# Performance work log

Hardware: AMD Instinct MI355X
Metric: run time of the kernel (lower is better)

Reference implementation:

```python
import jax, jax.numpy as jnp
import numpy as np


def _dot_prod_attention(h, enc):
    # h: (B,T,H), enc: (B,S,H) used as both keys and values
    att = jnp.einsum('bth,bsh->bts', h, enc)      # (B,T,S)
    att = jax.nn.softmax(att, axis=-1)
    ctx = jnp.einsum('bts,bsh->bth', att, enc)    # (B,T,H)
    return ctx, att


def setup_inputs() -> dict:
    key = jax.random.key(0)
    ks = jax.random.split(key, 7)
    B, T, S, St, H = 8, 1024, 1024, 512, 1024
    scale = 1.0 / np.sqrt(H)
    return {
        'output': jax.random.normal(ks[0], (B, T, H), dtype=jnp.float32),
        'sent': jax.random.normal(ks[1], (B, S, H), dtype=jnp.float32),
        'template': jax.random.normal(ks[2], (B, St, H), dtype=jnp.float32),
        'W_gate': jax.random.normal(ks[3], (H, 3 * H), dtype=jnp.float32) * scale,
        'W_sent': jax.random.normal(ks[4], (H, H), dtype=jnp.float32) * scale,
        'W_template': jax.random.normal(ks[5], (H, H), dtype=jnp.float32) * scale,
        'W_output': jax.random.normal(ks[6], (H, H), dtype=jnp.float32) * scale,
    }


def reference(output, sent, template, W_gate, W_sent, W_template, W_output):
    sent_ctx, sent_weight = _dot_prod_attention(output, sent)
    template_ctx, template_weight = _dot_prod_attention(output, template)

    cat = jnp.concatenate([sent_ctx, template_ctx, output], axis=-1)  # (B,T,3H)
    gate = jax.nn.sigmoid(jnp.einsum('btk,hk->bth', cat, W_gate))     # (B,T,H)

    fusion = ((1.0 - gate) * jnp.einsum('bth,kh->btk', sent_ctx, W_sent)
              + gate * jnp.einsum('bth,kh->btk', template_ctx, W_template)
              + jnp.einsum('bth,kh->btk', output, W_output))
    fusion = jnp.tanh(fusion)
    return fusion, sent_weight, template_weight
```

## Files before the change

### kernel.cpp

```cpp
#include <hip/hip_runtime.h>
#include <stdint.h>

typedef unsigned short u16;
typedef float    f32x4 __attribute__((ext_vector_type(4)));
typedef _Float16 f16x8 __attribute__((ext_vector_type(8)));
typedef _Float16 f16x4 __attribute__((ext_vector_type(4)));

__device__ __forceinline__ u16 f2h(float f) {
  _Float16 h = (_Float16)f;
  u16 u; __builtin_memcpy(&u, &h, 2); return u;
}
__device__ __forceinline__ float h2f(u16 u) {
  _Float16 h; __builtin_memcpy(&h, &u, 2); return (float)h;
}

__device__ __forceinline__ void mfma_f16(f32x4& c, f16x8 a, f16x8 b) {
  c = __builtin_amdgcn_mfma_f32_16x16x32_f16(a, b, c, 0, 0, 0);
}

__device__ __forceinline__ void g2l16(const u16* g, u16* l) {
  __builtin_amdgcn_global_load_lds((const __attribute__((address_space(1))) void*)g,
                                   (__attribute__((address_space(3))) void*)l,
                                   16, 0, 0);
}

__device__ __forceinline__ void xcd_batch(int& bx, int& by, int& bz) {
  const int gx = gridDim.x, gy = gridDim.y;
  const int n = gx * gy * gridDim.z;
  const int lin = blockIdx.x + gx * (blockIdx.y + gy * blockIdx.z);
  const int q = n >> 3;
  const int s = (lin & 7) * q + (lin >> 3);
  bx = s % gx;
  const int t2 = s / gx;
  by = t2 % gy;
  bz = t2 / gy;
}

__device__ __forceinline__ void xcd_col(int& bx, int& by) {
  const int gx = gridDim.x, gy = gridDim.y;
  const int n = gx * gy;
  const int cpx = n >> 3;
  const int lin = blockIdx.x + gx * blockIdx.y;
  const int s = (lin & 7) * cpx + (lin >> 3);
  bx = s / gy;
  by = s % gy;
}

struct alignas(8) US4 { u16 a, b, c, d; };

__global__ void k_conv_hilo(const float* __restrict__ src, u16* __restrict__ hi,
                            u16* __restrict__ lo, int n4) {
  int i = blockIdx.x * blockDim.x + threadIdx.x;
  int stride = gridDim.x * blockDim.x;
  for (; i < n4; i += stride) {
    float4 v = reinterpret_cast<const float4*>(src)[i];
    US4 h, l;
    h.a = f2h(v.x); l.a = f2h(v.x - h2f(h.a));
    h.b = f2h(v.y); l.b = f2h(v.y - h2f(h.b));
    h.c = f2h(v.z); l.c = f2h(v.z - h2f(h.c));
    h.d = f2h(v.w); l.d = f2h(v.w - h2f(h.d));
    reinterpret_cast<US4*>(hi)[i] = h;
    reinterpret_cast<US4*>(lo)[i] = l;
  }
}

__global__ void k_conv_w(const float* __restrict__ s_wg, const float* __restrict__ s_ws,
                         const float* __restrict__ s_wt, const float* __restrict__ s_wo,
                         u16* __restrict__ d_wg, u16* __restrict__ d_ws,
                         u16* __restrict__ d_wt, u16* __restrict__ d_wo) {
  constexpr int N1 = 786432;
  constexpr int N2 = 262144;
  constexpr int total = N1 + 3 * N2;
  int i = blockIdx.x * blockDim.x + threadIdx.x;
  int stride = gridDim.x * blockDim.x;
  for (; i < total; i += stride) {
    const float* s; u16* d; int j;
    if (i < N1)                { s = s_wg; d = d_wg; j = i; }
    else if (i < N1 + N2)      { s = s_ws; d = d_ws; j = i - N1; }
    else if (i < N1 + 2 * N2)  { s = s_wt; d = d_wt; j = i - N1 - N2; }
    else                       { s = s_wo; d = d_wo; j = i - N1 - 2 * N2; }
    float4 v = reinterpret_cast<const float4*>(s)[j];
    US4 h; h.a = f2h(v.x); h.b = f2h(v.y); h.c = f2h(v.z); h.d = f2h(v.w);
    reinterpret_cast<US4*>(d)[j] = h;
  }
}

__global__ __launch_bounds__(256)
void k_conv_T(const float* __restrict__ src, u16* __restrict__ dh, u16* __restrict__ dl,
              u16* __restrict__ dt, int R, int C) {
  __shared__ u16 t[32][33];
  const int b = blockIdx.z;
  const float* s = src + (size_t)b * R * C;
  u16* dhb = dh + (size_t)b * R * C;
  u16* dlb = dl + (size_t)b * R * C;
  u16* dtb = dt + (size_t)b * R * C;
  const int c0 = blockIdx.x * 32, r0 = blockIdx.y * 32;
  const int tx = threadIdx.x, ty = threadIdx.y;
#pragma unroll
  for (int j = ty; j < 32; j += 8) {
    const size_t idx = (size_t)(r0 + j) * C + (c0 + tx);
    float x = s[idx];
    u16 h = f2h(x);
    dhb[idx] = h;
    dlb[idx] = f2h(x - h2f(h));
    t[j][tx] = h;
  }
  __syncthreads();
#pragma unroll
  for (int j = ty; j < 32; j += 8)
    dtb[(size_t)(c0 + j) * R + (r0 + tx)] = t[tx][j];
}

template<int L>
__global__ __launch_bounds__(256)
void k_softmax(float* __restrict__ io, u16* __restrict__ pb) {
  const int lane = threadIdx.x & 63;
  const size_t r = (size_t)blockIdx.x * 4 + (threadIdx.x >> 6);
  float* row = io + r * L;
  u16* prow = pb + r * L;
  constexpr int NV = L / 64;
  float v[NV];
  float mx = -3.4e38f;
#pragma unroll
  for (int j = 0; j < NV; ++j) { v[j] = row[lane + j * 64]; mx = fmaxf(mx, v[j]); }
#pragma unroll
  for (int s = 32; s; s >>= 1) mx = fmaxf(mx, __shfl_xor(mx, s));
  float sum = 0.f;
#pragma unroll
  for (int j = 0; j < NV; ++j) { v[j] = __expf(v[j] - mx); sum += v[j]; }
#pragma unroll
  for (int s = 32; s; s >>= 1) sum += __shfl_xor(sum, s);
  const float inv = 1.f / sum;
#pragma unroll
  for (int j = 0; j < NV; ++j) {
    float pv = v[j] * inv;
    row[lane + j * 64] = pv;
    prow[lane + j * 64] = f2h(pv);
  }
}

struct TC { int wv, sr, sc, wm, wn, fr, kq; };

__device__ __forceinline__ TC make_tc(int tid) {
  TC t;
  const int lane = tid & 63;
  t.wv = tid >> 6;
  t.sr = lane >> 2;
  t.sc = (lane & 3) * 8;
  t.wm = t.wv >> 1;
  t.wn = t.wv & 1;
  t.fr = lane & 15;
  t.kq = (lane >> 4) * 8;
  return t;
}

constexpr int SUB = 128 * 32;

__device__ __forceinline__ void pass64(
    f32x4 (&acc)[16],
    const u16* __restrict__ A, int lda,
    const u16* __restrict__ B, int ldb,
    int K, u16* sA, u16* sB, const TC& t)
{
  const int nt = K / 64;
  auto stage = [&](int c, int k0) {
#pragma unroll
    for (int sub = 0; sub < 2; ++sub) {
      u16* dA = sA + c * (2 * SUB) + sub * SUB;
      u16* dB = sB + c * (2 * SUB) + sub * SUB;
      const u16* ar = A + (size_t)t.sr * lda + k0 + sub * 32 + t.sc;
      const u16* br = B + (size_t)t.sr * ldb + k0 + sub * 32 + t.sc;
      g2l16(ar + (size_t)(t.wv * 16) * lda, dA + (t.wv * 16) * 32);
      g2l16(ar + (size_t)((t.wv + 4) * 16) * lda, dA + ((t.wv + 4) * 16) * 32);
      g2l16(br + (size_t)(t.wv * 16) * ldb, dB + (t.wv * 16) * 32);
      g2l16(br + (size_t)((t.wv + 4) * 16) * ldb, dB + ((t.wv + 4) * 16) * 32);
    }
  };

  stage(0, 0);
  __syncthreads();
  int c = 0;
  for (int it = 0; it < nt; ++it) {
    if (it + 1 < nt) stage(c ^ 1, (it + 1) * 64);
#pragma unroll
    for (int sub = 0; sub < 2; ++sub) {
      const u16* bA = sA + c * (2 * SUB) + sub * SUB;
      const u16* bB = sB + c * (2 * SUB) + sub * SUB;
      f16x8 ah[4], bh[4];
#pragma unroll
      for (int i = 0; i < 4; ++i) {
        ah[i] = *reinterpret_cast<const f16x8*>(&bA[(t.wm * 64 + i * 16 + t.fr) * 32 + t.kq]);
        bh[i] = *reinterpret_cast<const f16x8*>(&bB[(t.wn * 64 + i * 16 + t.fr) * 32 + t.kq]);
      }
#pragma unroll
      for (int i = 0; i < 4; ++i)
#pragma unroll
        for (int j = 0; j < 4; ++j)
          mfma_f16(acc[i * 4 + j], ah[i], bh[j]);
    }
    __syncthreads();
    c ^= 1;
  }
}

__device__ __forceinline__ void pass32s(
    f32x4 (&acc)[16],
    const u16* __restrict__ A, const u16* __restrict__ Al, int lda,
    const u16* __restrict__ B, const u16* __restrict__ Bl, int ldb,
    int K, u16* sA, u16* sAl, u16* sB, u16* sBl, const TC& t)
{
  const int nt = K / 32;
  auto stage = [&](int c, int k0) {
    u16* dA = sA + c * SUB;  u16* dB = sB + c * SUB;
    u16* dAl = sAl + c * SUB; u16* dBl = sBl + c * SUB;
    const u16* ar = A + (size_t)t.sr * lda + k0 + t.sc;
    const u16* br = B + (size_t)t.sr * ldb + k0 + t.sc;
    const u16* alr = Al + (size_t)t.sr * lda + k0 + t.sc;
    const u16* blr = Bl + (size_t)t.sr * ldb + k0 + t.sc;
    g2l16(ar + (size_t)(t.wv * 16) * lda, dA + (t.wv * 16) * 32);
    g2l16(ar + (size_t)((t.wv + 4) * 16) * lda, dA + ((t.wv + 4) * 16) * 32);
    g2l16(br + (size_t)(t.wv * 16) * ldb, dB + (t.wv * 16) * 32);
    g2l16(br + (size_t)((t.wv + 4) * 16) * ldb, dB + ((t.wv + 4) * 16) * 32);
    g2l16(alr + (size_t)(t.wv * 16) * lda, dAl + (t.wv * 16) * 32);
    g2l16(alr + (size_t)((t.wv + 4) * 16) * lda, dAl + ((t.wv + 4) * 16) * 32);
    g2l16(blr + (size_t)(t.wv * 16) * ldb, dBl + (t.wv * 16) * 32);
    g2l16(blr + (size_t)((t.wv + 4) * 16) * ldb, dBl + ((t.wv + 4) * 16) * 32);
  };

  stage(0, 0);
  __syncthreads();
  int c = 0;
  for (int it = 0; it < nt; ++it) {
    if (it + 1 < nt) stage(c ^ 1, (it + 1) * 32);
    const u16* bA = sA + c * SUB;  const u16* bB = sB + c * SUB;
    const u16* bAl = sAl + c * SUB; const u16* bBl = sBl + c * SUB;
    f16x8 ah[4], bh[4], al[4], bl[4];
#pragma unroll
    for (int i = 0; i < 4; ++i) {
      ah[i] = *reinterpret_cast<const f16x8*>(&bA[(t.wm * 64 + i * 16 + t.fr) * 32 + t.kq]);
      bh[i] = *reinterpret_cast<const f16x8*>(&bB[(t.wn * 64 + i * 16 + t.fr) * 32 + t.kq]);
      al[i] = *reinterpret_cast<const f16x8*>(&bAl[(t.wm * 64 + i * 16 + t.fr) * 32 + t.kq]);
      bl[i] = *reinterpret_cast<const f16x8*>(&bBl[(t.wn * 64 + i * 16 + t.fr) * 32 + t.kq]);
    }
#pragma unroll
    for (int i = 0; i < 4; ++i)
#pragma unroll
      for (int j = 0; j < 4; ++j) {
        mfma_f16(acc[i * 4 + j], ah[i], bh[j]);
        mfma_f16(acc[i * 4 + j], al[i], bh[j]);
        mfma_f16(acc[i * 4 + j], ah[i], bl[j]);
      }
    __syncthreads();
    c ^= 1;
  }
}

__global__ __launch_bounds__(256, 2)
void k_logits(const u16* __restrict__ Ah, const u16* __restrict__ Al,
              const u16* __restrict__ Bh, const u16* __restrict__ Bl,
              long long strB, float* __restrict__ Cf, int ldc, long long strC)
{
  __shared__ __align__(16) u16 sA[2 * SUB], sB[2 * SUB], sAl[2 * SUB], sBl[2 * SUB];
  int bx, by, bz;
  xcd_batch(bx, by, bz);
  const TC t = make_tc(threadIdx.x);

  const size_t aoff = (size_t)bz * (1024 * 1024) + (size_t)by * 128 * 1024;
  const size_t boff = (size_t)bz * strB + (size_t)bx * 128 * 1024;

  f32x4 acc[16];
#pragma unroll
  for (int i = 0; i < 16; ++i) acc[i] = f32x4{0.f, 0.f, 0.f, 0.f};

  pass32s(acc, Ah + aoff, Al + aoff, 1024, Bh + boff, Bl + boff, 1024, 1024,
          sA, sAl, sB, sBl, t);

  const size_t cbse = (size_t)bz * strC;
  const int row0 = by * 128 + t.wm * 64;
  const int col0 = bx * 128 + t.wn * 64;
  const int fq = ((threadIdx.x & 63) >> 4) * 4;
#pragma unroll
  for (int i = 0; i < 4; ++i)
#pragma unroll
    for (int j = 0; j < 4; ++j) {
      const int c = col0 + j * 16 + t.fr;
#pragma unroll
      for (int q = 0; q < 4; ++q)
        Cf[cbse + (size_t)(row0 + i * 16 + fq + q) * ldc + c] = acc[i * 4 + j][q];
    }
}

__global__ __launch_bounds__(256, 2)
void k_pv(const u16* __restrict__ A, const u16* __restrict__ Bt, int ld,
          long long strA, long long strB, u16* __restrict__ Cb, long long strC)
{
  __shared__ __align__(16) u16 sA[2 * 2 * SUB], sB[2 * 2 * SUB];
  int bx, by, bz;
  xcd_batch(bx, by, bz);
  const TC t = make_tc(threadIdx.x);

  f32x4 acc[16];
#pragma unroll
  for (int i = 0; i < 16; ++i) acc[i] = f32x4{0.f, 0.f, 0.f, 0.f};

  pass64(acc, A + (size_t)bz * strA + (size_t)by * 128 * ld, ld,
         Bt + (size_t)bz * strB + (size_t)bx * 128 * ld, ld, ld, sA, sB, t);

  const size_t cbse = (size_t)bz * strC;
  const int row0 = by * 128 + t.wm * 64;
  const int col0 = bx * 128 + t.wn * 64;
  const int fq = ((threadIdx.x & 63) >> 4) * 4;
#pragma unroll
  for (int i = 0; i < 4; ++i)
#pragma unroll
    for (int j = 0; j < 4; ++j) {
      const int c = col0 + j * 16 + t.fr;
#pragma unroll
      for (int q = 0; q < 4; ++q)
        Cb[cbse + (size_t)(row0 + i * 16 + fq + q) * 1024 + c] = f2h(acc[i * 4 + j][q]);
    }
}

__global__ __launch_bounds__(256, 2)
void k_fusion4(const u16* __restrict__ ctx_s, const u16* __restrict__ ctx_t,
               const u16* __restrict__ outh,
               const u16* __restrict__ Wg, const u16* __restrict__ Ws,
               const u16* __restrict__ Wt, const u16* __restrict__ Wo,
               float* __restrict__ fus)
{
  constexpr int H = 1024;
  __shared__ __align__(16) u16 sA[2 * 2 * SUB], sB[2 * 2 * SUB];

  int bx, by;
  xcd_col(bx, by);
  const TC t = make_tc(threadIdx.x);

  const size_t aoff = (size_t)by * 128 * H;
  const int row0 = by * 128 + t.wm * 64;
  const int col0 = bx * 128 + t.wn * 64;
  const int fq = ((threadIdx.x & 63) >> 4) * 4;

  f32x4 acc[16];
#pragma unroll
  for (int i = 0; i < 16; ++i) acc[i] = f32x4{0.f, 0.f, 0.f, 0.f};

  const u16* As[3] = {ctx_s, ctx_t, outh};
  for (int s = 0; s < 3; ++s)
    pass64(acc, As[s] + aoff, H, Wg + (size_t)bx * 128 * (3 * H) + s * H, 3 * H, H,
           sA, sB, t);
  f16x4 gh[16];
#pragma unroll
  for (int f = 0; f < 16; ++f)
#pragma unroll
    for (int q = 0; q < 4; ++q)
      gh[f][q] = (_Float16)(1.f / (1.f + __expf(-acc[f][q])));

#pragma unroll
  for (int i = 0; i < 16; ++i) acc[i] = f32x4{0.f, 0.f, 0.f, 0.f};
  pass64(acc, ctx_s + aoff, H, Ws + (size_t)bx * 128 * H, H, H, sA, sB, t);
  f32x4 S[16];
#pragma unroll
  for (int i = 0; i < 16; ++i) { S[i] = acc[i]; acc[i] = f32x4{0.f, 0.f, 0.f, 0.f}; }

  pass64(acc, ctx_t + aoff, H, Wt + (size_t)bx * 128 * H, H, H, sA, sB, t);
#pragma unroll
  for (int f = 0; f < 16; ++f)
#pragma unroll
    for (int q = 0; q < 4; ++q) {
      const float gv = (float)gh[f][q];
      const float sv = S[f][q];
      S[f][q] = sv + gv * (acc[f][q] - sv);
    }
#pragma unroll
  for (int i = 0; i < 16; ++i) acc[i] = f32x4{0.f, 0.f, 0.f, 0.f};

  pass64(acc, outh + aoff, H, Wo + (size_t)bx * 128 * H, H, H, sA, sB, t);
#pragma unroll
  for (int i = 0; i < 4; ++i)
#pragma unroll
    for (int j = 0; j < 4; ++j) {
      const int c = col0 + j * 16 + t.fr;
#pragma unroll
      for (int q = 0; q < 4; ++q) {
        const int r = row0 + i * 16 + fq + q;
        float x = S[i * 4 + j][q] + acc[i * 4 + j][q];
        float ax = fabsf(x);
        float e = __expf(-2.f * ax);
        float th = (1.f - e) / (1.f + e);
        fus[(size_t)r * H + c] = copysignf(th, x);
      }
    }
}

extern "C" void kernel_launch(void* const* d_in, const int* in_sizes, int n_in,
                              void* d_out, int out_size, void* d_ws, size_t ws_size,
                              hipStream_t stream) {
  (void)in_sizes; (void)n_in; (void)out_size; (void)ws_size;
  constexpr int B = 8, T = 1024, S = 1024, St = 512, H = 1024;
  constexpr long long BTH = (long long)B * T * H;
  constexpr long long BSH = (long long)B * S * H;
  constexpr long long BStH = (long long)B * St * H;
  constexpr long long BTS = (long long)B * T * S;
  constexpr long long BTSt = (long long)B * T * St;
  constexpr long long TH = (long long)T * H;

  const float* in_out  = (const float*)d_in[0];
  const float* in_sent = (const float*)d_in[1];
  const float* in_tmpl = (const float*)d_in[2];
  const float* in_Wg   = (const float*)d_in[3];
  const float* in_Ws   = (const float*)d_in[4];
  const float* in_Wt   = (const float*)d_in[5];
  const float* in_Wo   = (const float*)d_in[6];

  float* fus = (float*)d_out;
  float* sw  = fus + BTH;
  float* tw  = sw + BTS;

  char* p = (char*)d_ws;
  auto take = [&](long long bytes) { char* q = p; p += bytes; return q; };
  u16* out_h   = (u16*)take(BTH * 2);
  u16* out_lo  = (u16*)take(BTH * 2);
  u16* sent_h  = (u16*)take(BSH * 2);
  u16* sent_lo = (u16*)take(BSH * 2);
  u16* tmpl_h  = (u16*)take(BStH * 2);
  u16* tmpl_lo = (u16*)take(BStH * 2);
  u16* sentT   = (u16*)take(BSH * 2);
  u16* tmplT   = (u16*)take(BStH * 2);
  u16* Wg_h    = (u16*)take((long long)3 * H * H * 2);
  u16* Ws_h    = (u16*)take((long long)H * H * 2);
  u16* Wt_h    = (u16*)take((long long)H * H * 2);
  u16* Wo_h    = (u16*)take((long long)H * H * 2);
  u16* Ps      = (u16*)take(BTS * 2);
  u16* Pt      = (u16*)take(BTSt * 2);

  u16* ctx_s = sent_h;
  u16* ctx_t = sent_lo;

  dim3 thr(256);

  k_conv_hilo<<<2048, 256, 0, stream>>>(in_out, out_h, out_lo, (int)(BTH / 4));
  k_conv_w<<<1024, 256, 0, stream>>>(in_Wg, in_Ws, in_Wt, in_Wo, Wg_h, Ws_h, Wt_h, Wo_h);
  k_conv_T<<<dim3(H / 32, S / 32, B), dim3(32, 8), 0, stream>>>(in_sent, sent_h, sent_lo, sentT, S, H);
  k_conv_T<<<dim3(H / 32, St / 32, B), dim3(32, 8), 0, stream>>>(in_tmpl, tmpl_h, tmpl_lo, tmplT, St, H);

  k_logits<<<dim3(S / 128, T / 128, B), thr, 0, stream>>>(
      out_h, out_lo, sent_h, sent_lo, (long long)S * H, sw, S, (long long)T * S);
  k_logits<<<dim3(St / 128, T / 128, B), thr, 0, stream>>>(
      out_h, out_lo, tmpl_h, tmpl_lo, (long long)St * H, tw, St, (long long)T * St);

  k_softmax<1024><<<(B * T) / 4, 256, 0, stream>>>(sw, Ps);
  k_softmax<512><<<(B * T) / 4, 256, 0, stream>>>(tw, Pt);

  k_pv<<<dim3(H / 128, T / 128, B), thr, 0, stream>>>(
      Ps, sentT, S, (long long)T * S, (long long)H * S, ctx_s, TH);
  k_pv<<<dim3(H / 128, T / 128, B), thr, 0, stream>>>(
      Pt, tmplT, St, (long long)T * St, (long long)H * St, ctx_t, TH);

  k_fusion4<<<dim3(H / 128, (B * T) / 128), thr, 0, stream>>>(
      ctx_s, ctx_t, out_h, Wg_h, Ws_h, Wt_h, Wo_h, fus);
}
```

Before: 401.2 us.

## Share A-tile loads between gate and projection GEMMs in fusion kernel

The fusion kernel now streams each A operand (ctx_s, ctx_t, output) once and multiplies it against both the matching gate-weight slice and the matching projection weight, keeping two accumulator sets. This replaces six sequential passes, which reloaded each A tile twice, with three dual-B passes, cutting A-side global and LDS traffic. The sigmoid is moved to the epilogue and the intermediate S/T projections are held as fp16 to save registers. The cost is higher register pressure from the doubled accumulators and a smaller K-step (32 instead of 64), and the fp16 storage of the intermediates loses some precision. The swizzle helpers are also unified into a single 3D version.

```diff
diff --git a/kernel.cpp b/kernel.cpp
--- a/kernel.cpp
+++ b/kernel.cpp
@@ -24,7 +24,7 @@
                                    16, 0, 0);
 }
 
-__device__ __forceinline__ void xcd_batch(int& bx, int& by, int& bz) {
+__device__ __forceinline__ void xcd_swz(int& bx, int& by, int& bz) {
   const int gx = gridDim.x, gy = gridDim.y;
   const int n = gx * gy * gridDim.z;
   const int lin = blockIdx.x + gx * (blockIdx.y + gy * blockIdx.z);
@@ -34,16 +34,6 @@
   const int t2 = s / gx;
   by = t2 % gy;
   bz = t2 / gy;
-}
-
-__device__ __forceinline__ void xcd_col(int& bx, int& by) {
-  const int gx = gridDim.x, gy = gridDim.y;
-  const int n = gx * gy;
-  const int cpx = n >> 3;
-  const int lin = blockIdx.x + gx * blockIdx.y;
-  const int s = (lin & 7) * cpx + (lin >> 3);
-  bx = s / gy;
-  by = s % gy;
 }
 
 struct alignas(8) US4 { u16 a, b, c, d; };
@@ -255,6 +245,68 @@
   }
 }
 
+__device__ __forceinline__ void pass32d(
+    f32x4 (&accZ)[16], f32x4 (&accW)[16],
+    const u16* __restrict__ A, int lda,
+    const u16* __restrict__ B0, int ldb0,
+    const u16* __restrict__ B1, int ldb1,
+    int K, u16* sA, u16* sB0, u16* sB1, const TC& t)
+{
+  const int nt = K / 32;
+  auto stage = [&](int c, int k0) {
+    u16* dA = sA + c * SUB;
+    u16* d0 = sB0 + c * SUB;
+    u16* d1 = sB1 + c * SUB;
+    const u16* ar = A + (size_t)t.sr * lda + k0 + t.sc;
+    const u16* b0 = B0 + (size_t)t.sr * ldb0 + k0 + t.sc;
+    const u16* b1 = B1 + (size_t)t.sr * ldb1 + k0 + t.sc;
+    g2l16(ar + (size_t)(t.wv * 16) * lda, dA + (t.wv * 16) * 32);
+    g2l16(ar + (size_t)((t.wv + 4) * 16) * lda, dA + ((t.wv + 4) * 16) * 32);
+    g2l16(b0 + (size_t)(t.wv * 16) * ldb0, d0 + (t.wv * 16) * 32);
+    g2l16(b0 + (size_t)((t.wv + 4) * 16) * ldb0, d0 + ((t.wv + 4) * 16) * 32);
+    g2l16(b1 + (size_t)(t.wv * 16) * ldb1, d1 + (t.wv * 16) * 32);
+    g2l16(b1 + (size_t)((t.wv + 4) * 16) * ldb1, d1 + ((t.wv + 4) * 16) * 32);
+  };
+
+  stage(0, 0);
+  __syncthreads();
+  int c = 0;
+  for (int it = 0; it < nt; ++it) {
+    if (it + 1 < nt) stage(c ^ 1, (it + 1) * 32);
+    const u16* bA = sA + c * SUB;
+    f16x8 ah[4];
+#pragma unroll
+    for (int i = 0; i < 4; ++i)
+      ah[i] = *reinterpret_cast<const f16x8*>(&bA[(t.wm * 64 + i * 16 + t.fr) * 32 + t.kq]);
+    {
+      const u16* b0 = sB0 + c * SUB;
+      f16x8 bh[4];
+#pragma unroll
+      for (int j = 0; j < 4; ++j)
+        bh[j] = *reinterpret_cast<const f16x8*>(&b0[(t.wn * 64 + j * 16 + t.fr) * 32 + t.kq]);
+#pragma unroll
+      for (int i = 0; i < 4; ++i)
+#pragma unroll
+        for (int j = 0; j < 4; ++j)
+          mfma_f16(accZ[i * 4 + j], ah[i], bh[j]);
+    }
+    {
+      const u16* b1 = sB1 + c * SUB;
+      f16x8 bh[4];
+#pragma unroll
+      for (int j = 0; j < 4; ++j)
+        bh[j] = *reinterpret_cast<const f16x8*>(&b1[(t.wn * 64 + j * 16 + t.fr) * 32 + t.kq]);
+#pragma unroll
+      for (int i = 0; i < 4; ++i)
+#pragma unroll
+        for (int j = 0; j < 4; ++j)
+          mfma_f16(accW[i * 4 + j], ah[i], bh[j]);
+    }
+    __syncthreads();
+    c ^= 1;
+  }
+}
+
 __global__ __launch_bounds__(256, 2)
 void k_logits(const u16* __restrict__ Ah, const u16* __restrict__ Al,
               const u16* __restrict__ Bh, const u16* __restrict__ Bl,
@@ -262,7 +314,7 @@
 {
   __shared__ __align__(16) u16 sA[2 * SUB], sB[2 * SUB], sAl[2 * SUB], sBl[2 * SUB];
   int bx, by, bz;
-  xcd_batch(bx, by, bz);
+  xcd_swz(bx, by, bz);
   const TC t = make_tc(threadIdx.x);
 
   const size_t aoff = (size_t)bz * (1024 * 1024) + (size_t)by * 128 * 1024;
@@ -296,7 +348,7 @@
 {
   __shared__ __align__(16) u16 sA[2 * 2 * SUB], sB[2 * 2 * SUB];
   int bx, by, bz;
-  xcd_batch(bx, by, bz);
+  xcd_swz(bx, by, bz);
   const TC t = make_tc(threadIdx.x);
 
   f32x4 acc[16];
@@ -329,61 +381,61 @@
                float* __restrict__ fus)
 {
   constexpr int H = 1024;
-  __shared__ __align__(16) u16 sA[2 * 2 * SUB], sB[2 * 2 * SUB];
-
-  int bx, by;
-  xcd_col(bx, by);
+  __shared__ __align__(16) u16 sA[2 * SUB], sB0[2 * SUB], sB1[2 * SUB];
+
+  int bx, by, bz;
+  xcd_swz(bx, by, bz);
   const TC t = make_tc(threadIdx.x);
 
   const size_t aoff = (size_t)by * 128 * H;
+  const size_t wgoff = (size_t)bx * 128 * (3 * H);
   const int row0 = by * 128 + t.wm * 64;
   const int col0 = bx * 128 + t.wn * 64;
   const int fq = ((threadIdx.x & 63) >> 4) * 4;
 
-  f32x4 acc[16];
-#pragma unroll
-  for (int i = 0; i < 16; ++i) acc[i] = f32x4{0.f, 0.f, 0.f, 0.f};
-
-  const u16* As[3] = {ctx_s, ctx_t, outh};
-  for (int s = 0; s < 3; ++s)
-    pass64(acc, As[s] + aoff, H, Wg + (size_t)bx * 128 * (3 * H) + s * H, 3 * H, H,
-           sA, sB, t);
-  f16x4 gh[16];
-#pragma unroll
-  for (int f = 0; f < 16; ++f)
-#pragma unroll
-    for (int q = 0; q < 4; ++q)
-      gh[f][q] = (_Float16)(1.f / (1.f + __expf(-acc[f][q])));
-
-#pragma unroll
-  for (int i = 0; i < 16; ++i) acc[i] = f32x4{0.f, 0.f, 0.f, 0.f};
-  pass64(acc, ctx_s + aoff, H, Ws + (size_t)bx * 128 * H, H, H, sA, sB, t);
-  f32x4 S[16];
-#pragma unroll
-  for (int i = 0; i < 16; ++i) { S[i] = acc[i]; acc[i] = f32x4{0.f, 0.f, 0.f, 0.f}; }
-
-  pass64(acc, ctx_t + aoff, H, Wt + (size_t)bx * 128 * H, H, H, sA, sB, t);
-#pragma unroll
-  for (int f = 0; f < 16; ++f)
-#pragma unroll
-    for (int q = 0; q < 4; ++q) {
-      const float gv = (float)gh[f][q];
-      const float sv = S[f][q];
-      S[f][q] = sv + gv * (acc[f][q] - sv);
-    }
-#pragma unroll
-  for (int i = 0; i < 16; ++i) acc[i] = f32x4{0.f, 0.f, 0.f, 0.f};
-
-  pass64(acc, outh + aoff, H, Wo + (size_t)bx * 128 * H, H, H, sA, sB, t);
+  f32x4 accZ[16], accW[16];
+#pragma unroll
+  for (int i = 0; i < 16; ++i) {
+    accZ[i] = f32x4{0.f, 0.f, 0.f, 0.f};
+    accW[i] = f32x4{0.f, 0.f, 0.f, 0.f};
+  }
+
+  pass32d(accZ, accW, ctx_s + aoff, H, Wg + wgoff, 3 * H,
+          Ws + (size_t)bx * 128 * H, H, H, sA, sB0, sB1, t);
+  f16x4 S16[16];
+#pragma unroll
+  for (int f = 0; f < 16; ++f) {
+#pragma unroll
+    for (int q = 0; q < 4; ++q) S16[f][q] = (_Float16)accW[f][q];
+    accW[f] = f32x4{0.f, 0.f, 0.f, 0.f};
+  }
+
+  pass32d(accZ, accW, ctx_t + aoff, H, Wg + wgoff + H, 3 * H,
+          Wt + (size_t)bx * 128 * H, H, H, sA, sB0, sB1, t);
+  f16x4 T16[16];
+#pragma unroll
+  for (int f = 0; f < 16; ++f) {
+#pragma unroll
+    for (int q = 0; q < 4; ++q) T16[f][q] = (_Float16)accW[f][q];
+    accW[f] = f32x4{0.f, 0.f, 0.f, 0.f};
+  }
+
+  pass32d(accZ, accW, outh + aoff, H, Wg + wgoff + 2 * H, 3 * H,
+          Wo + (size_t)bx * 128 * H, H, H, sA, sB0, sB1, t);
+
 #pragma unroll
   for (int i = 0; i < 4; ++i)
 #pragma unroll
     for (int j = 0; j < 4; ++j) {
+      const int f = i * 4 + j;
       const int c = col0 + j * 16 + t.fr;
 #pragma unroll
       for (int q = 0; q < 4; ++q) {
         const int r = row0 + i * 16 + fq + q;
-        float x = S[i * 4 + j][q] + acc[i * 4 + j][q];
+        const float g = 1.f / (1.f + __expf(-accZ[f][q]));
+        const float sv = (float)S16[f][q];
+        const float tv = (float)T16[f][q];
+        float x = sv + g * (tv - sv) + accW[f][q];
         float ax = fabsf(x);
         float e = __expf(-2.f * ax);
         float th = (1.f - e) / (1.f + e);
```

After: 352.5 us. -12.2%, faster.
